# Performance work log

Measured on AMD Instinct MI355X. Metric: run time of the kernel, lower is better.

Reference implementation:

```python
import jax, jax.numpy as jnp
import numpy as np

THRESHOLD = 0.045
TAU = 20.0
N = 1048576
H = 128


def setup_inputs() -> dict:
    key = jax.random.key(0)
    ks = jax.random.split(key, 7)
    x = jax.random.normal(ks[0], (N, 1), dtype=jnp.float32)
    s1 = 1.0  # 1/sqrt(fan_in=1)
    s2 = 1.0 / np.sqrt(H).astype(np.float32)
    W1 = jax.random.uniform(ks[1], (H, 1), jnp.float32, -s1, s1)
    b1 = jax.random.uniform(ks[2], (H,), jnp.float32, -s1, s1)
    W2 = jax.random.uniform(ks[3], (H, H), jnp.float32, -s2, s2)
    b2 = jax.random.uniform(ks[4], (H,), jnp.float32, -s2, s2)
    W3 = jax.random.uniform(ks[5], (1, H), jnp.float32, -s2, s2)
    b3 = jax.random.uniform(ks[6], (1,), jnp.float32, -s2, s2)
    return {"x": x, "W1": W1, "b1": b1, "W2": W2, "b2": b2, "W3": W3, "b3": b3}


def reference(x, W1, b1, W2, b2, W3, b3):
    n = x.shape[0]
    # threshold-gated event mask (mask[0] forced active, as in original)
    diff = jnp.abs(x - jnp.roll(x, 1, axis=0))[:, 0]
    mask = (diff > THRESHOLD).at[0].set(True)
    # tiny MLP; computed densely — values at non-active rows are never read
    # (output gathers only last-active rows), so the math matches the
    # original's gather-then-MLP exactly.
    h = jax.nn.relu(x @ W1.T + b1)        # [N, H]
    h = jax.nn.relu(h @ W2.T + b2)        # [N, H]
    y = h @ W3.T + b3                     # [N, 1]
    t = jnp.arange(n, dtype=jnp.float32)
    # last active time <= i  (cumsum(mask)-1 indexing into active rows is
    # equivalent to gathering at the last active position)
    last_t = jax.lax.cummax(jnp.where(mask, t, jnp.float32(0.0)))  # [N]
    last_idx = last_t.astype(jnp.int32)
    decay = jnp.exp(-(t - last_t) / TAU)[:, None]  # [N, 1]
    output = y[last_idx] * decay
    n_active = mask.sum(dtype=jnp.int32)
    return output, n_active
```

## Files before the change

kernel.cpp:

```cpp
#include <hip/hip_runtime.h>
#include <math.h>


#define THRESH   0.045f
#define NH       128
#define TSZ      8192
#define GMIN     -6.0f
#define GMAX     6.0f
#define TPB      256
#define ITEMS    2
#define CHUNK    (TPB * ITEMS)
#define NSCAN    2048
#define NTBLK    256
#define POISON32 0xAAAAAAAAu

__global__ __launch_bounds__(TPB) void kT(const float* __restrict__ W1,
                                          const float* __restrict__ b1,
                                          const float* __restrict__ W2,
                                          const float* __restrict__ b2,
                                          const float* __restrict__ W3,
                                          const float* __restrict__ b3,
                                          float* __restrict__ table) {
  __shared__ float w2s[NH * NH];
  const int t = threadIdx.x, b = blockIdx.x;
  {
    const float4* src = (const float4*)W2;
    float4* dst = (float4*)w2s;
    #pragma unroll
    for (int i = 0; i < (NH * NH / 4) / TPB; ++i)
      dst[t + i * TPB] = src[t + i * TPB];
  }
  __syncthreads();

  const int p  = t & 15;
  const int e0 = b * 32 + (t >> 4) * 2;
  const float step = (GMAX - GMIN) * (1.0f / (float)(TSZ - 1));
  const float xv0 = GMIN + step * (float)e0;
  const float xv1 = xv0 + step;

  float h10[8], h11[8];
  #pragma unroll
  for (int c = 0; c < 2; ++c) {
    #pragma unroll
    for (int r = 0; r < 4; ++r) {
      const int k = 4 * (p + 16 * c) + r;
      const float w = W1[k], bb = b1[k];
      h10[c * 4 + r] = fmaxf(fmaf(xv0, w, bb), 0.0f);
      h11[c * 4 + r] = fmaxf(fmaf(xv1, w, bb), 0.0f);
    }
  }
  const bool hi = (p & 8) != 0;
  float y = 0.0f;
  const float b3v = b3[0];
  #pragma unroll 4
  for (int j = 0; j < NH; ++j) {
    const float* row = &w2s[j * NH];
    float a0 = 0.f, a1 = 0.f, c0 = 0.f, c1 = 0.f;
    #pragma unroll
    for (int c = 0; c < 2; ++c) {
      const float4 w = *(const float4*)&row[4 * (p + 16 * c)];
      a0 = fmaf(h10[c * 4 + 0], w.x, a0);
      a1 = fmaf(h10[c * 4 + 1], w.y, a1);
      a0 = fmaf(h10[c * 4 + 2], w.z, a0);
      a1 = fmaf(h10[c * 4 + 3], w.w, a1);
      c0 = fmaf(h11[c * 4 + 0], w.x, c0);
      c1 = fmaf(h11[c * 4 + 1], w.y, c1);
      c0 = fmaf(h11[c * 4 + 2], w.z, c0);
      c1 = fmaf(h11[c * 4 + 3], w.w, c1);
    }
    const float s0 = a0 + a1, s1 = c0 + c1;
    float u = hi ? s1 : s0;
    float v = hi ? s0 : s1;
    v = __shfl_xor(v, 8);
    u += v;
    u += __shfl_xor(u, 1);
    u += __shfl_xor(u, 2);
    u += __shfl_xor(u, 4);
    const float h2 = fmaxf(u + b2[j], 0.0f);
    y = fmaf(h2, W3[j], y);
  }
  if ((p & 7) == 0) table[e0 + (p >> 3)] = y + b3v;
}

__global__ __launch_bounds__(TPB) void kS(const float* __restrict__ x, int n,
                                          const float* __restrict__ table,
                                          unsigned int* __restrict__ cnts,
                                          float* __restrict__ out) {
  __shared__ int swl[4], swc[4], sred[4];
  __shared__ int sgx;
  const int t = threadIdx.x, b = blockIdx.x;
  const int lane = t & 63, wv = t >> 6;
  const int base = b * CHUNK + t * ITEMS;

  float xs[ITEMS];
  const bool full = (base + ITEMS) <= n;
  if (full) {
    const float2 v = *(const float2*)(x + base);
    xs[0] = v.x; xs[1] = v.y;
  } else {
    #pragma unroll
    for (int it = 0; it < ITEMS; ++it)
      xs[it] = (base + it < n) ? x[base + it] : 0.0f;
  }
  float prev = (base > 0 && base <= n) ? x[base - 1] : 0.0f;
  unsigned m = 0; int tl = -1; int cnt = 0;
  #pragma unroll
  for (int it = 0; it < ITEMS; ++it) {
    const int i = base + it;
    if (i < n) {
      const bool act = (i == 0) || (fabsf(xs[it] - prev) > THRESH);
      if (act) { tl = i; ++cnt; m |= (1u << it); }
      prev = xs[it];
    }
  }

  int incl = tl;
  #pragma unroll
  for (int off = 1; off < 64; off <<= 1) {
    const int v = __shfl_up(incl, off);
    if (lane >= off) incl = max(incl, v);
  }
  int wsum = cnt;
  #pragma unroll
  for (int off = 1; off < 64; off <<= 1) wsum += __shfl_xor(wsum, off);
  if (lane == 63) swl[wv] = incl;
  if (lane == 0)  swc[wv] = wsum;

  if (wv == 0) {
    int g = -1;
    if (b > 0) {
      int ws = b * CHUNK - 64;
      for (;;) {
        const int i = ws + lane;
        const float xi = x[i];
        const float xp = (i > 0) ? x[i - 1] : 0.0f;
        const bool act = (i == 0) || (fabsf(xi - xp) > THRESH);
        const unsigned long long bal = __ballot(act);
        if (bal) { g = ws + 63 - (int)__builtin_clzll(bal); break; }
        ws -= 64;
      }
    }
    if (lane == 0) sgx = g;
  }
  __syncthreads();

  const int exclW = __shfl_up(incl, 1);
  int run = sgx;
  #pragma unroll
  for (int w = 0; w < 4; ++w) if (w < wv) run = max(run, swl[w]);
  if (lane > 0) run = max(run, exclW);

  if (t == 0) {
    const int bcnt = swc[0] + swc[1] + swc[2] + swc[3];
    __hip_atomic_store(&cnts[b], (unsigned)(bcnt + 1),
                       __ATOMIC_RELAXED, __HIP_MEMORY_SCOPE_AGENT);
  }

  const float invstep = (float)(TSZ - 1) / (GMAX - GMIN);
  if (full) {
    float o[ITEMS];
    #pragma unroll
    for (int it = 0; it < ITEMS; ++it) {
      const int i = base + it;
      const bool act = (m >> it) & 1u;
      if (act) run = i;
      const float xj = act ? xs[it] : x[run];
      const float u = (xj - GMIN) * invstep;
      int i0 = (int)u;
      i0 = max(0, min(i0, TSZ - 2));
      const float f = u - (float)i0;
      const float t0 = table[i0], t1 = table[i0 + 1];
      o[it] = fmaf(f, t1 - t0, t0) * __expf((float)(run - i) * 0.05f);
    }
    float2 ov = { o[0], o[1] };
    *(float2*)(out + base) = ov;
  } else {
    #pragma unroll
    for (int it = 0; it < ITEMS; ++it) {
      const int i = base + it;
      if (i >= n) break;
      const bool act = (m >> it) & 1u;
      if (act) run = i;
      const float xj = act ? xs[it] : x[run];
      const float u = (xj - GMIN) * invstep;
      int i0 = (int)u;
      i0 = max(0, min(i0, TSZ - 2));
      const float f = u - (float)i0;
      const float t0 = table[i0], t1 = table[i0 + 1];
      out[i] = fmaf(f, t1 - t0, t0) * __expf((float)(run - i) * 0.05f);
    }
  }

  if (b == 0) {
    int v = 0;
    #pragma unroll
    for (int s8 = 0; s8 < NSCAN / TPB; ++s8) {
      const int idx = t + s8 * TPB;
      unsigned c;
      for (;;) {
        c = __hip_atomic_load(&cnts[idx], __ATOMIC_RELAXED,
                              __HIP_MEMORY_SCOPE_AGENT);
        if (c != POISON32) break;
        __builtin_amdgcn_s_sleep(1);
      }
      v += (int)c - 1;
    }
    #pragma unroll
    for (int off = 1; off < 64; off <<= 1) v += __shfl_xor(v, off);
    if (lane == 0) sred[wv] = v;
    __syncthreads();
    if (t == 0) out[n] = (float)(sred[0] + sred[1] + sred[2] + sred[3]);
  }
}

extern "C" void kernel_launch(void* const* d_in, const int* in_sizes, int n_in,
                              void* d_out, int out_size, void* d_ws, size_t ws_size,
                              hipStream_t stream) {
  const float* x  = (const float*)d_in[0];
  const float* W1 = (const float*)d_in[1];
  const float* b1 = (const float*)d_in[2];
  const float* W2 = (const float*)d_in[3];
  const float* b2 = (const float*)d_in[4];
  const float* W3 = (const float*)d_in[5];
  const float* b3 = (const float*)d_in[6];
  float* out = (float*)d_out;
  const int n = in_sizes[0];

  char* w = (char*)d_ws;
  float* table = (float*)w;
  unsigned int* cnts = (unsigned int*)(w + TSZ * 4);

  kT<<<NTBLK, TPB, 0, stream>>>(W1, b1, W2, b2, W3, b3, table);
  kS<<<NSCAN, TPB, 0, stream>>>(x, n, table, cnts, out);
}
```

Before: 90.89 us.

## Use DPP reductions, read W2 from global, and last-block ticket count reduction

The table kernel drops its 64KB LDS staging of W2 and reads rows straight from global/L2, and it swaps shuffle-xor reductions for DPP row ops, moving the writer lane to 7. The scan kernel replaces block 0 spin-waiting on per-block counters with striped atomic adds plus a ticket counter, so the last-arriving block sums the partials. This removes a serial spin-wait on block 0 and LDS occupancy limits, but it relies on the workspace being pre-poisoned to 0xAA bytes as the implicit initial value.

Result: slower. 124.5 us (+37.0%).

```diff
diff --git a/kernel.cpp b/kernel.cpp
--- a/kernel.cpp
+++ b/kernel.cpp
@@ -14,6 +14,15 @@
 #define NTBLK    256
 #define POISON32 0xAAAAAAAAu
 
+#define ROW_SHR1 0x111
+#define ROW_SHR2 0x112
+#define ROW_SHR4 0x114
+#define ROW_ROR8 0x128
+
+#define DPP_ADD(u, v, ctrl)                                                  \
+  ((u) + __builtin_bit_cast(float, __builtin_amdgcn_update_dpp(              \
+             0, __builtin_bit_cast(int, (v)), (ctrl), 0xf, 0xf, true)))
+
 __global__ __launch_bounds__(TPB) void kT(const float* __restrict__ W1,
                                           const float* __restrict__ b1,
                                           const float* __restrict__ W2,
@@ -21,17 +30,7 @@
                                           const float* __restrict__ W3,
                                           const float* __restrict__ b3,
                                           float* __restrict__ table) {
-  __shared__ float w2s[NH * NH];
   const int t = threadIdx.x, b = blockIdx.x;
-  {
-    const float4* src = (const float4*)W2;
-    float4* dst = (float4*)w2s;
-    #pragma unroll
-    for (int i = 0; i < (NH * NH / 4) / TPB; ++i)
-      dst[t + i * TPB] = src[t + i * TPB];
-  }
-  __syncthreads();
-
   const int p  = t & 15;
   const int e0 = b * 32 + (t >> 4) * 2;
   const float step = (GMAX - GMIN) * (1.0f / (float)(TSZ - 1));
@@ -54,7 +53,7 @@
   const float b3v = b3[0];
   #pragma unroll 4
   for (int j = 0; j < NH; ++j) {
-    const float* row = &w2s[j * NH];
+    const float* row = &W2[j * NH];
     float a0 = 0.f, a1 = 0.f, c0 = 0.f, c1 = 0.f;
     #pragma unroll
     for (int c = 0; c < 2; ++c) {
@@ -71,22 +70,22 @@
     const float s0 = a0 + a1, s1 = c0 + c1;
     float u = hi ? s1 : s0;
     float v = hi ? s0 : s1;
-    v = __shfl_xor(v, 8);
-    u += v;
-    u += __shfl_xor(u, 1);
-    u += __shfl_xor(u, 2);
-    u += __shfl_xor(u, 4);
+    u = DPP_ADD(u, v, ROW_ROR8);
+    u = DPP_ADD(u, u, ROW_SHR1);
+    u = DPP_ADD(u, u, ROW_SHR2);
+    u = DPP_ADD(u, u, ROW_SHR4);
     const float h2 = fmaxf(u + b2[j], 0.0f);
     y = fmaf(h2, W3[j], y);
   }
-  if ((p & 7) == 0) table[e0 + (p >> 3)] = y + b3v;
+  if ((p & 7) == 7) table[e0 + (p >> 3)] = y + b3v;
 }
 
 __global__ __launch_bounds__(TPB) void kS(const float* __restrict__ x, int n,
                                           const float* __restrict__ table,
-                                          unsigned int* __restrict__ cnts,
+                                          unsigned int* __restrict__ gsum,
+                                          unsigned int* __restrict__ gticket,
                                           float* __restrict__ out) {
-  __shared__ int swl[4], swc[4], sred[4];
+  __shared__ int swl[4], swc[4];
   __shared__ int sgx;
   const int t = threadIdx.x, b = blockIdx.x;
   const int lane = t & 63, wv = t >> 6;
@@ -150,10 +149,15 @@
   for (int w = 0; w < 4; ++w) if (w < wv) run = max(run, swl[w]);
   if (lane > 0) run = max(run, exclW);
 
+  bool winner = false;
   if (t == 0) {
-    const int bcnt = swc[0] + swc[1] + swc[2] + swc[3];
-    __hip_atomic_store(&cnts[b], (unsigned)(bcnt + 1),
-                       __ATOMIC_RELAXED, __HIP_MEMORY_SCOPE_AGENT);
+    const unsigned bcnt = (unsigned)(swc[0] + swc[1] + swc[2] + swc[3]);
+    __hip_atomic_fetch_add(&gsum[(b & 15) * 16], bcnt,
+                           __ATOMIC_RELAXED, __HIP_MEMORY_SCOPE_AGENT);
+    const unsigned tk = __hip_atomic_fetch_add(gticket, 1u,
+                                               __ATOMIC_ACQ_REL,
+                                               __HIP_MEMORY_SCOPE_AGENT);
+    winner = (tk == POISON32 + (unsigned)(NSCAN - 1));
   }
 
   const float invstep = (float)(TSZ - 1) / (GMAX - GMIN);
@@ -191,25 +195,14 @@
     }
   }
 
-  if (b == 0) {
-    int v = 0;
-    #pragma unroll
-    for (int s8 = 0; s8 < NSCAN / TPB; ++s8) {
-      const int idx = t + s8 * TPB;
-      unsigned c;
-      for (;;) {
-        c = __hip_atomic_load(&cnts[idx], __ATOMIC_RELAXED,
-                              __HIP_MEMORY_SCOPE_AGENT);
-        if (c != POISON32) break;
-        __builtin_amdgcn_s_sleep(1);
-      }
-      v += (int)c - 1;
-    }
-    #pragma unroll
-    for (int off = 1; off < 64; off <<= 1) v += __shfl_xor(v, off);
-    if (lane == 0) sred[wv] = v;
-    __syncthreads();
-    if (t == 0) out[n] = (float)(sred[0] + sred[1] + sred[2] + sred[3]);
+  if (winner) {
+    unsigned s = 0;
+    #pragma unroll
+    for (int k = 0; k < 16; ++k)
+      s += __hip_atomic_load(&gsum[k * 16], __ATOMIC_RELAXED,
+                             __HIP_MEMORY_SCOPE_AGENT);
+    s -= 16u * POISON32;
+    out[n] = (float)(int)s;
   }
 }
 
@@ -228,8 +221,9 @@
 
   char* w = (char*)d_ws;
   float* table = (float*)w;
-  unsigned int* cnts = (unsigned int*)(w + TSZ * 4);
+  unsigned int* gsum    = (unsigned int*)(w + TSZ * 4);
+  unsigned int* gticket = (unsigned int*)(w + TSZ * 4 + 1024);
 
   kT<<<NTBLK, TPB, 0, stream>>>(W1, b1, W2, b2, W3, b3, table);
-  kS<<<NSCAN, TPB, 0, stream>>>(x, n, table, cnts, out);
+  kS<<<NSCAN, TPB, 0, stream>>>(x, n, table, gsum, gticket, out);
 }
```
